# Performance work log

Hardware: AMD Instinct MI355X
Metric: run time of the kernel (lower is better)

## Reference

```python
import jax, jax.numpy as jnp
import numpy as np

K = 2048      # codebook_size
D = 64        # codebook_dim
B = 32
T = 4096
W = 0.99      # codebook_loss_weight (EMA decay)
THRESH = 1.0  # discard_vec_threshold


def setup_inputs() -> dict:
    key = jax.random.key(0)
    k1, k2 = jax.random.split(key, 2)
    x = jax.random.normal(k1, (B, D, T), jnp.float32)
    codebook = jax.random.normal(k2, (K, D), jnp.float32)
    codebook_avg = codebook.copy()
    vector_usage = jnp.ones((K,), jnp.float32)
    perm = jnp.arange(B * T, dtype=jnp.int32)  # deterministic stand-in for randperm
    return dict(x=x, codebook=codebook, codebook_avg=codebook_avg,
                vector_usage=vector_usage, perm=perm)


def reference(x, codebook, codebook_avg, vector_usage, perm):
    Bv, E, Tv = x.shape
    sg = jax.lax.stop_gradient
    # preprocess: [B, E, T] -> [N, E]
    xf = jnp.transpose(x, (0, 2, 1)).reshape(-1, E)
    N = xf.shape[0]
    x_norm = jnp.linalg.norm(xf - jnp.mean(xf)) / np.sqrt(N * E)
    # squared euclidean distances [N, K]
    d = (jnp.sum(xf * xf, axis=-1, keepdims=True)
         - 2.0 * (xf @ codebook.T)
         + jnp.sum(codebook * codebook, axis=-1))
    idx = jnp.argmin(d, axis=-1)            # [N]
    fit = jnp.mean(jnp.min(d, axis=-1))
    q = codebook[idx]                       # [N, E] gather
    # --- update_codebook (torch.no_grad) ---
    cb_sum = jax.ops.segment_sum(sg(xf), idx, num_segments=K)          # onehot @ x
    counts = jax.ops.segment_sum(jnp.ones((N,), xf.dtype), idx, num_segments=K)
    new_avg = W * sg(codebook_avg) + (1.0 - W) * cb_sum
    new_usage = W * sg(vector_usage) + (1.0 - W) * counts
    keep = (new_usage >= THRESH).astype(xf.dtype)[:, None]
    random_shift = sg(xf)[perm][:K]
    new_codebook = keep * (new_avg / new_usage[:, None]) + (1.0 - keep) * random_shift
    vector_prob = counts / jnp.sum(counts)
    entropy = -jnp.sum(vector_prob * jnp.log(vector_prob + 1e-8))
    codebook_diff = jnp.linalg.norm(new_codebook - sg(codebook)) / np.sqrt(K * E)
    # --- commitment loss + straight-through ---
    commit_loss = jnp.sum((sg(q) - xf) ** 2) / (N * E)
    out = xf + sg(q - xf)
    out = jnp.transpose(out.reshape(Bv, Tv, E), (0, 2, 1))  # [B, E, T]
    return (out, commit_loss, fit, x_norm, new_codebook, new_avg, new_usage,
            entropy, codebook_diff)
```

## Files before the change

### kernel.cpp

```cpp
#include <hip/hip_runtime.h>
#include <math.h>

#define OUT_X      0
#define OUT_COMMIT 8388608
#define OUT_FIT    8388609
#define OUT_XNORM  8388610
#define OUT_NCB    8388611
#define OUT_NAVG   (8388611 + 131072)
#define OUT_NUSE   (8388611 + 262144)
#define OUT_ENT    (8388611 + 264192)
#define OUT_CBDIFF (8388611 + 264193)

#define WS_DACC    0
#define WS_COUNTS  64
#define WS_CBSUM   8256
#define WS_CURS    532544
#define WS_XN2     540736
#define WS_IDX     1065024
#define WS_CN2H    1589312
#define WS_SORTED  1597504
#define WS_CHI     2121792
#define WS_CLO     2383936
#define WS_ZERO_BYTES 532544

#define LO_SCALE5  32.0f

typedef _Float16 f16x8_t __attribute__((ext_vector_type(8)));
typedef float f32x16_t __attribute__((ext_vector_type(16)));

__global__ __launch_bounds__(256) void kern_prep_x(
    const float* __restrict__ x, float* __restrict__ xt,
    float* __restrict__ xn2, double* __restrict__ dacc)
{
    __shared__ __align__(16) float Xs[64][128];
    __shared__ float tmpA[4], tmpB[4];
    const int tid = threadIdx.x;
    const int n0 = blockIdx.x * 128;
    const int b = n0 >> 12, t0 = n0 & 4095;
    const float* xb = x + ((size_t)b << 18) + t0;
#pragma unroll
    for (int i = 0; i < 8; ++i) {
        int c = i * 256 + tid;
        int e = c >> 5, v4 = c & 31;
        float4 f = *(const float4*)(xb + ((size_t)e << 12) + (v4 << 2));
        *(float4*)&Xs[e][v4 << 2] = f;
    }
    __syncthreads();
    const int q = tid & 3, r0 = tid >> 2;
    float s1t = 0.f, s2t = 0.f;
#pragma unroll
    for (int h = 0; h < 2; ++h) {
        int r = r0 + (h << 6);
        float s2 = 0.f;
#pragma unroll
        for (int j = 0; j < 4; ++j) {
            int e = q * 16 + j * 4;
            float4 f = make_float4(Xs[e][r], Xs[e + 1][r], Xs[e + 2][r], Xs[e + 3][r]);
            *(float4*)(xt + (((size_t)(n0 + r)) << 6) + e) = f;
            s1t += f.x + f.y + f.z + f.w;
            s2 += f.x * f.x + f.y * f.y + f.z * f.z + f.w * f.w;
        }
        s2t += s2;
        float s2q = s2 + __shfl_xor(s2, 1, 64);
        s2q += __shfl_xor(s2q, 2, 64);
        if (q == 0) xn2[n0 + r] = s2q;
    }
    float rs = s1t, r2 = s2t;
#pragma unroll
    for (int m = 32; m >= 1; m >>= 1) {
        rs += __shfl_xor(rs, m, 64);
        r2 += __shfl_xor(r2, m, 64);
    }
    if ((tid & 63) == 0) { tmpA[tid >> 6] = rs; tmpB[tid >> 6] = r2; }
    __syncthreads();
    if (tid == 0) {
        atomicAdd(&dacc[0], (double)(tmpA[0] + tmpA[1] + tmpA[2] + tmpA[3]));
        atomicAdd(&dacc[1], (double)(tmpB[0] + tmpB[1] + tmpB[2] + tmpB[3]));
    }
}

__global__ __launch_bounds__(256) void kern_prep_cb(
    const float* __restrict__ cb, _Float16* __restrict__ chi,
    _Float16* __restrict__ clo, float* __restrict__ cn2h)
{
    __shared__ float Cs[128][68];
    const int tid = threadIdx.x;
    const int c0 = blockIdx.x * 128;
#pragma unroll
    for (int i = 0; i < 8; ++i) {
        int li = i * 256 + tid;
        int code = li >> 4, d4 = li & 15;
        float4 f = *(const float4*)(cb + (((size_t)(c0 + code)) << 6) + (d4 << 2));
        Cs[code][d4 * 4 + 0] = f.x; Cs[code][d4 * 4 + 1] = f.y;
        Cs[code][d4 * 4 + 2] = f.z; Cs[code][d4 * 4 + 3] = f.w;
    }
    __syncthreads();
    const int w = tid >> 6, lane = tid & 63;
    const int cl = (w << 5) + (lane & 31);
    const int g = lane >> 5;
    const int ktg = blockIdx.x * 4 + w;
#pragma unroll
    for (int s = 0; s < 4; ++s) {
        f16x8_t hh, ll;
#pragma unroll
        for (int i = 0; i < 8; ++i) {
            int k = 16 * s + 4 * g + (i & 3) + 8 * (i >> 2);
            float v = Cs[cl][k];
            _Float16 h = (_Float16)v;
            hh[i] = h;
            ll[i] = (_Float16)((v - (float)h) * LO_SCALE5);
        }
        *(f16x8_t*)(chi + (((size_t)(ktg * 4 + s)) << 9) + lane * 8) = hh;
        *(f16x8_t*)(clo + (((size_t)(ktg * 4 + s)) << 9) + lane * 8) = ll;
    }
    if (tid < 128) {
        float s = 0.f;
#pragma unroll
        for (int k = 0; k < 64; ++k) { float v = Cs[tid][k]; s = fmaf(v, v, s); }
        cn2h[c0 + tid] = -0.5f * s;
    }
}

__global__ __launch_bounds__(256) void kern_argmin_mfma(
    const float* __restrict__ xt, const float* __restrict__ cn2h,
    const _Float16* __restrict__ chi, const _Float16* __restrict__ clo,
    const float* __restrict__ xn2, int* __restrict__ idxb,
    unsigned* __restrict__ counts, double* __restrict__ dacc)
{
    const int tid = threadIdx.x;
    const int w = tid >> 6, lane = tid & 63;
    const int n0 = blockIdx.x * 128 + w * 32;
    const int l31 = lane & 31, g = lane >> 5;

    f16x8_t ahi[4], alo5[4];
    {
        const float* xr = xt + ((size_t)(n0 + l31) << 6) + 4 * g;
#pragma unroll
        for (int s = 0; s < 4; ++s) {
            float4 p = *(const float4*)(xr + 16 * s);
            float4 q = *(const float4*)(xr + 16 * s + 8);
            float vals[8] = {p.x, p.y, p.z, p.w, q.x, q.y, q.z, q.w};
#pragma unroll
            for (int i = 0; i < 8; ++i) {
                _Float16 h = (_Float16)vals[i];
                ahi[s][i] = h;
                alo5[s][i] = (_Float16)((vals[i] - (float)h) * LO_SCALE5);
            }
        }
    }
    float bestm[16]; int besti[16];
#pragma unroll
    for (int r = 0; r < 16; ++r) { bestm[r] = -INFINITY; besti[r] = 0; }

    const _Float16* chiL = chi + lane * 8;
    const _Float16* cloL = clo + lane * 8;

    f16x8_t bhA[4], blA[4], bhB[4], blB[4];
    float cvA, cvB;
#pragma unroll
    for (int s = 0; s < 4; ++s) {
        bhA[s] = *(const f16x8_t*)(chiL + ((0 * 4 + s) << 9));
        blA[s] = *(const f16x8_t*)(cloL + ((0 * 4 + s) << 9));
    }
    cvA = cn2h[l31];

#define ITER(t_, bhC, blC, cvC, bhN, blN, cvN) do {                          \
    if ((t_) + 1 < 64) {                                                     \
        _Pragma("unroll")                                                    \
        for (int s = 0; s < 4; ++s) {                                        \
            bhN[s] = *(const f16x8_t*)(chiL + ((((t_) + 1) * 4 + s) << 9));  \
            blN[s] = *(const f16x8_t*)(cloL + ((((t_) + 1) * 4 + s) << 9));  \
        }                                                                    \
        cvN = cn2h[(((t_) + 1) << 5) + l31];                                 \
    }                                                                        \
    f32x16_t a;                                                              \
    _Pragma("unroll")                                                        \
    for (int r = 0; r < 16; ++r) a[r] = 0.f;                                 \
    __builtin_amdgcn_s_setprio(1);                                           \
    _Pragma("unroll")                                                        \
    for (int s = 0; s < 4; ++s)                                              \
        a = __builtin_amdgcn_mfma_f32_32x32x16_f16(ahi[s], blC[s], a, 0, 0, 0); \
    _Pragma("unroll")                                                        \
    for (int s = 0; s < 4; ++s)                                              \
        a = __builtin_amdgcn_mfma_f32_32x32x16_f16(alo5[s], bhC[s], a, 0, 0, 0); \
    _Pragma("unroll")                                                        \
    for (int r = 0; r < 16; ++r) a[r] = fmaf(a[r], 0.03125f, cvC);           \
    _Pragma("unroll")                                                        \
    for (int s = 0; s < 4; ++s)                                              \
        a = __builtin_amdgcn_mfma_f32_32x32x16_f16(ahi[s], bhC[s], a, 0, 0, 0); \
    __builtin_amdgcn_s_setprio(0);                                           \
    _Pragma("unroll")                                                        \
    for (int r = 0; r < 16; ++r)                                             \
        if (a[r] > bestm[r]) { bestm[r] = a[r]; besti[r] = (t_); }           \
} while (0)

    for (int t = 0; t < 64; t += 2) {
        ITER(t, bhA, blA, cvA, bhB, blB, cvB);
        ITER(t + 1, bhB, blB, cvB, bhA, blA, cvA);
    }
#undef ITER

    float fs = 0.f;
#pragma unroll
    for (int r = 0; r < 16; ++r) {
        float mv = bestm[r]; int mi = (besti[r] << 5) + l31;
#pragma unroll
        for (int m = 1; m < 32; m <<= 1) {
            float ov = __shfl_xor(mv, m, 64);
            int oi = __shfl_xor(mi, m, 64);
            if (ov > mv || (ov == mv && oi < mi)) { mv = ov; mi = oi; }
        }
        if (l31 == 0) {
            int row = (r & 3) + 8 * (r >> 2) + 4 * g;
            int n = n0 + row;
            idxb[n] = mi;
            atomicAdd(&counts[mi], 1u);
            fs += xn2[n] - 2.f * mv;
        }
    }
    if (l31 == 0) atomicAdd(&dacc[2], (double)fs);
}

__global__ void kern_scan(const unsigned* __restrict__ counts, unsigned* __restrict__ curs) {
    __shared__ unsigned wtot[4];
    const int tid = threadIdx.x;
    const int base = tid * 8;
    unsigned s[8]; unsigned tot = 0;
#pragma unroll
    for (int j = 0; j < 8; ++j) { s[j] = counts[base + j]; tot += s[j]; }
    unsigned v = tot;
    const int lane = tid & 63;
#pragma unroll
    for (int d = 1; d < 64; d <<= 1) {
        unsigned o = (unsigned)__shfl_up((int)v, d, 64);
        if (lane >= d) v += o;
    }
    if (lane == 63) wtot[tid >> 6] = v;
    __syncthreads();
    unsigned wbase = 0;
    for (int w = 0; w < (tid >> 6); ++w) wbase += wtot[w];
    unsigned run = wbase + v - tot;
#pragma unroll
    for (int j = 0; j < 8; ++j) { curs[base + j] = run; run += s[j]; }
}

__global__ void kern_scatter(const int* __restrict__ idxb, unsigned* __restrict__ curs,
                             unsigned* __restrict__ sorted) {
    const int n = blockIdx.x * 256 + threadIdx.x;
    int k = idxb[n];
    unsigned pos = atomicAdd(&curs[k], 1u);
    sorted[pos] = ((unsigned)k << 17) | (unsigned)n;
}

__global__ __launch_bounds__(256) void kern_chunk_reduce(
    const float* __restrict__ xt, const unsigned* __restrict__ sorted,
    float* __restrict__ cb_sum)
{
    const int tid = threadIdx.x;
    const int w = tid >> 6, lane = tid & 63;
    const int base = blockIdx.x * 256 + w * 64;
    int kcur = (int)(sorted[base] >> 17);
    float acc = 0.f;
#pragma unroll 4
    for (int it = 0; it < 16; ++it) {
        uint4 p = *(const uint4*)&sorted[base + it * 4];
        float v0 = xt[((size_t)(p.x & 0x1FFFFu) << 6) + lane];
        float v1 = xt[((size_t)(p.y & 0x1FFFFu) << 6) + lane];
        float v2 = xt[((size_t)(p.z & 0x1FFFFu) << 6) + lane];
        float v3 = xt[((size_t)(p.w & 0x1FFFFu) << 6) + lane];
        int k0 = (int)(p.x >> 17), k1 = (int)(p.y >> 17);
        int k2 = (int)(p.z >> 17), k3 = (int)(p.w >> 17);
        if (k0 != kcur) { atomicAdd(&cb_sum[(kcur << 6) + lane], acc); kcur = k0; acc = 0.f; }
        acc += v0;
        if (k1 != kcur) { atomicAdd(&cb_sum[(kcur << 6) + lane], acc); kcur = k1; acc = 0.f; }
        acc += v1;
        if (k2 != kcur) { atomicAdd(&cb_sum[(kcur << 6) + lane], acc); kcur = k2; acc = 0.f; }
        acc += v2;
        if (k3 != kcur) { atomicAdd(&cb_sum[(kcur << 6) + lane], acc); kcur = k3; acc = 0.f; }
        acc += v3;
    }
    atomicAdd(&cb_sum[(kcur << 6) + lane], acc);
}

__global__ __launch_bounds__(256) void kern_update(
    const float* __restrict__ cb_sum, const unsigned* __restrict__ counts,
    const float* __restrict__ cb, const float* __restrict__ cba,
    const float* __restrict__ usage, const int* __restrict__ perm,
    const float* __restrict__ xt, float* __restrict__ out,
    double* __restrict__ dacc)
{
    const int tid = threadIdx.x;
    const int i = blockIdx.x * 256 + tid;
    const int k = i >> 6, e = i & 63;
    float na = 0.99f * cba[i] + 0.01f * cb_sum[i];
    float nu = 0.99f * usage[k] + 0.01f * (float)counts[k];
    float ncb = (nu >= 1.0f) ? (na / nu)
                             : xt[((size_t)perm[k] << 6) + e];
    out[OUT_NAVG + i] = na;
    out[OUT_NCB + i] = ncb;
    if (e == 0) out[OUT_NUSE + k] = nu;
    float d = ncb - cb[i];
    float dd = d * d;
#pragma unroll
    for (int m = 32; m >= 1; m >>= 1) dd += __shfl_xor(dd, m, 64);
    if (e == 0) atomicAdd(&dacc[4], (double)dd);
}

__global__ __launch_bounds__(256) void kern_out(
    const float* __restrict__ x, const float* __restrict__ cb,
    const int* __restrict__ idxb, float* __restrict__ out,
    double* __restrict__ dacc) {
    __shared__ float tmp[4];
    const int tid = threadIdx.x;
    const int n0 = blockIdx.x * 256 + (tid & 63) * 4;
    const int ec = tid >> 6;
    const int b = n0 >> 12, t = n0 & 4095;
    int4 k4 = *(const int4*)(idxb + n0);
    const float* xb = x + ((size_t)b << 18) + t;
    float* ob = out + OUT_X + ((size_t)b << 18) + t;
    float cl = 0.f;
#pragma unroll
    for (int j = 0; j < 16; ++j) {
        int e = ec * 16 + j;
        float4 xv = *(const float4*)(xb + ((size_t)e << 12));
        float q0 = cb[((size_t)k4.x << 6) + e], q1 = cb[((size_t)k4.y << 6) + e];
        float q2 = cb[((size_t)k4.z << 6) + e], q3 = cb[((size_t)k4.w << 6) + e];
        float r0 = q0 - xv.x, r1 = q1 - xv.y, r2 = q2 - xv.z, r3 = q3 - xv.w;
        cl += r0 * r0 + r1 * r1 + r2 * r2 + r3 * r3;
        *(float4*)(ob + ((size_t)e << 12)) = make_float4(q0, q1, q2, q3);
    }
#pragma unroll
    for (int m = 32; m >= 1; m >>= 1) cl += __shfl_xor(cl, m, 64);
    if ((tid & 63) == 0) tmp[tid >> 6] = cl;
    __syncthreads();
    if (tid == 0) atomicAdd(&dacc[3], (double)(tmp[0] + tmp[1] + tmp[2] + tmp[3]));
}

__global__ void kern_scalars(const unsigned* __restrict__ counts,
                             const double* __restrict__ dacc, float* __restrict__ out) {
    __shared__ float tmp[4];
    __shared__ float totalSh;
    const int tid = threadIdx.x;
    float c = 0.f;
    for (int k = tid; k < 2048; k += 256) c += (float)counts[k];
#pragma unroll
    for (int m = 32; m >= 1; m >>= 1) c += __shfl_xor(c, m, 64);
    if ((tid & 63) == 0) tmp[tid >> 6] = c;
    __syncthreads();
    if (tid == 0) totalSh = tmp[0] + tmp[1] + tmp[2] + tmp[3];
    __syncthreads();
    const float total = totalSh;
    float ent = 0.f;
    for (int k = tid; k < 2048; k += 256) {
        float p = (float)counts[k] / total;
        ent -= p * logf(p + 1e-8f);
    }
#pragma unroll
    for (int m = 32; m >= 1; m >>= 1) ent += __shfl_xor(ent, m, 64);
    __syncthreads();
    if ((tid & 63) == 0) tmp[tid >> 6] = ent;
    __syncthreads();
    if (tid == 0) {
        float entropy = tmp[0] + tmp[1] + tmp[2] + tmp[3];
        out[OUT_COMMIT] = (float)(dacc[3] / 8388608.0);
        out[OUT_FIT]    = (float)(dacc[2] / 131072.0);
        double nd = 8388608.0;
        double var = dacc[1] - dacc[0] * dacc[0] / nd;
        if (var < 0.0) var = 0.0;
        out[OUT_XNORM] = (float)(sqrt(var) / sqrt(nd));
        out[OUT_ENT] = entropy;
        out[OUT_CBDIFF] = (float)(sqrt(dacc[4]) / sqrt(131072.0));
    }
}

extern "C" void kernel_launch(void* const* d_in, const int* in_sizes, int n_in,
                              void* d_out, int out_size, void* d_ws, size_t ws_size,
                              hipStream_t stream) {
    const float* x     = (const float*)d_in[0];
    const float* cb    = (const float*)d_in[1];
    const float* cba   = (const float*)d_in[2];
    const float* usage = (const float*)d_in[3];
    const int*   perm  = (const int*)d_in[4];
    float* out = (float*)d_out;
    char* ws = (char*)d_ws;
    double*    dacc   = (double*)(ws + WS_DACC);
    unsigned*  counts = (unsigned*)(ws + WS_COUNTS);
    float*     cbsum  = (float*)(ws + WS_CBSUM);
    unsigned*  curs   = (unsigned*)(ws + WS_CURS);
    float*     xn2    = (float*)(ws + WS_XN2);
    int*       idxb   = (int*)(ws + WS_IDX);
    float*     cn2h   = (float*)(ws + WS_CN2H);
    unsigned*  sorted = (unsigned*)(ws + WS_SORTED);
    _Float16*  chi    = (_Float16*)(ws + WS_CHI);
    _Float16*  clo    = (_Float16*)(ws + WS_CLO);
    float*     xt     = out + OUT_X;

    hipMemsetAsync(ws, 0, WS_ZERO_BYTES, stream);
    kern_prep_x<<<1024, 256, 0, stream>>>(x, xt, xn2, dacc);
    kern_prep_cb<<<16, 256, 0, stream>>>(cb, chi, clo, cn2h);
    kern_argmin_mfma<<<1024, 256, 0, stream>>>(xt, cn2h, chi, clo, xn2, idxb, counts, dacc);
    kern_scan<<<1, 256, 0, stream>>>(counts, curs);
    kern_scatter<<<512, 256, 0, stream>>>(idxb, curs, sorted);
    kern_chunk_reduce<<<512, 256, 0, stream>>>(xt, sorted, cbsum);
    kern_update<<<512, 256, 0, stream>>>(cbsum, counts, cb, cba, usage, perm, xt, out, dacc);
    kern_out<<<512, 256, 0, stream>>>(x, cb, idxb, out, dacc);
    kern_scalars<<<1, 256, 0, stream>>>(counts, dacc, out);
}
```

Before: 310.5 us.

## Process two row blocks per wave in argmin and derive commit loss from fit

The argmin kernel now gives each wave 64 rows as two 32-row MFMA tiles. Each tile shares the same codebook hi/lo fragments, so codebook loads are halved per row. The grid is halved, and the lo-fragment prefetch moves to the middle of the MFMA chain. The two prep kernels merge into one launch split by block index. The commit loss is computed from the summed minimum distance, since that equals the sum of squared residuals, so the output kernel no longer reads x. Costs: more registers per wave and lower occupancy, and commit now inherits the rounding error of the split-fp16 distance.

```diff
diff --git a/kernel.cpp b/kernel.cpp
--- a/kernel.cpp
+++ b/kernel.cpp
@@ -28,96 +28,95 @@
 typedef _Float16 f16x8_t __attribute__((ext_vector_type(8)));
 typedef float f32x16_t __attribute__((ext_vector_type(16)));
 
-__global__ __launch_bounds__(256) void kern_prep_x(
+__global__ __launch_bounds__(256) void kern_prep(
     const float* __restrict__ x, float* __restrict__ xt,
-    float* __restrict__ xn2, double* __restrict__ dacc)
-{
-    __shared__ __align__(16) float Xs[64][128];
-    __shared__ float tmpA[4], tmpB[4];
-    const int tid = threadIdx.x;
-    const int n0 = blockIdx.x * 128;
-    const int b = n0 >> 12, t0 = n0 & 4095;
-    const float* xb = x + ((size_t)b << 18) + t0;
-#pragma unroll
-    for (int i = 0; i < 8; ++i) {
-        int c = i * 256 + tid;
-        int e = c >> 5, v4 = c & 31;
-        float4 f = *(const float4*)(xb + ((size_t)e << 12) + (v4 << 2));
-        *(float4*)&Xs[e][v4 << 2] = f;
-    }
-    __syncthreads();
-    const int q = tid & 3, r0 = tid >> 2;
-    float s1t = 0.f, s2t = 0.f;
-#pragma unroll
-    for (int h = 0; h < 2; ++h) {
-        int r = r0 + (h << 6);
-        float s2 = 0.f;
-#pragma unroll
-        for (int j = 0; j < 4; ++j) {
-            int e = q * 16 + j * 4;
-            float4 f = make_float4(Xs[e][r], Xs[e + 1][r], Xs[e + 2][r], Xs[e + 3][r]);
-            *(float4*)(xt + (((size_t)(n0 + r)) << 6) + e) = f;
-            s1t += f.x + f.y + f.z + f.w;
-            s2 += f.x * f.x + f.y * f.y + f.z * f.z + f.w * f.w;
-        }
-        s2t += s2;
-        float s2q = s2 + __shfl_xor(s2, 1, 64);
-        s2q += __shfl_xor(s2q, 2, 64);
-        if (q == 0) xn2[n0 + r] = s2q;
-    }
-    float rs = s1t, r2 = s2t;
-#pragma unroll
-    for (int m = 32; m >= 1; m >>= 1) {
-        rs += __shfl_xor(rs, m, 64);
-        r2 += __shfl_xor(r2, m, 64);
-    }
-    if ((tid & 63) == 0) { tmpA[tid >> 6] = rs; tmpB[tid >> 6] = r2; }
-    __syncthreads();
-    if (tid == 0) {
-        atomicAdd(&dacc[0], (double)(tmpA[0] + tmpA[1] + tmpA[2] + tmpA[3]));
-        atomicAdd(&dacc[1], (double)(tmpB[0] + tmpB[1] + tmpB[2] + tmpB[3]));
-    }
-}
-
-__global__ __launch_bounds__(256) void kern_prep_cb(
+    float* __restrict__ xn2, double* __restrict__ dacc,
     const float* __restrict__ cb, _Float16* __restrict__ chi,
     _Float16* __restrict__ clo, float* __restrict__ cn2h)
 {
-    __shared__ float Cs[128][68];
-    const int tid = threadIdx.x;
-    const int c0 = blockIdx.x * 128;
-#pragma unroll
-    for (int i = 0; i < 8; ++i) {
-        int li = i * 256 + tid;
-        int code = li >> 4, d4 = li & 15;
-        float4 f = *(const float4*)(cb + (((size_t)(c0 + code)) << 6) + (d4 << 2));
-        Cs[code][d4 * 4 + 0] = f.x; Cs[code][d4 * 4 + 1] = f.y;
-        Cs[code][d4 * 4 + 2] = f.z; Cs[code][d4 * 4 + 3] = f.w;
-    }
-    __syncthreads();
-    const int w = tid >> 6, lane = tid & 63;
-    const int cl = (w << 5) + (lane & 31);
-    const int g = lane >> 5;
-    const int ktg = blockIdx.x * 4 + w;
-#pragma unroll
-    for (int s = 0; s < 4; ++s) {
-        f16x8_t hh, ll;
+    __shared__ __align__(16) char smem[128 * 68 * 4];
+    __shared__ float tmpA[4], tmpB[4];
+    const int tid = threadIdx.x;
+    if (blockIdx.x < 1024) {
+        float (*Xs)[128] = (float(*)[128])smem;
+        const int n0 = blockIdx.x * 128;
+        const int b = n0 >> 12, t0 = n0 & 4095;
+        const float* xb = x + ((size_t)b << 18) + t0;
 #pragma unroll
         for (int i = 0; i < 8; ++i) {
-            int k = 16 * s + 4 * g + (i & 3) + 8 * (i >> 2);
-            float v = Cs[cl][k];
-            _Float16 h = (_Float16)v;
-            hh[i] = h;
-            ll[i] = (_Float16)((v - (float)h) * LO_SCALE5);
-        }
-        *(f16x8_t*)(chi + (((size_t)(ktg * 4 + s)) << 9) + lane * 8) = hh;
-        *(f16x8_t*)(clo + (((size_t)(ktg * 4 + s)) << 9) + lane * 8) = ll;
-    }
-    if (tid < 128) {
-        float s = 0.f;
-#pragma unroll
-        for (int k = 0; k < 64; ++k) { float v = Cs[tid][k]; s = fmaf(v, v, s); }
-        cn2h[c0 + tid] = -0.5f * s;
+            int c = i * 256 + tid;
+            int e = c >> 5, v4 = c & 31;
+            float4 f = *(const float4*)(xb + ((size_t)e << 12) + (v4 << 2));
+            *(float4*)&Xs[e][v4 << 2] = f;
+        }
+        __syncthreads();
+        const int q = tid & 3, r0 = tid >> 2;
+        float s1t = 0.f, s2t = 0.f;
+#pragma unroll
+        for (int h = 0; h < 2; ++h) {
+            int r = r0 + (h << 6);
+            float s2 = 0.f;
+#pragma unroll
+            for (int j = 0; j < 4; ++j) {
+                int e = q * 16 + j * 4;
+                float4 f = make_float4(Xs[e][r], Xs[e + 1][r], Xs[e + 2][r], Xs[e + 3][r]);
+                *(float4*)(xt + (((size_t)(n0 + r)) << 6) + e) = f;
+                s1t += f.x + f.y + f.z + f.w;
+                s2 += f.x * f.x + f.y * f.y + f.z * f.z + f.w * f.w;
+            }
+            s2t += s2;
+            float s2q = s2 + __shfl_xor(s2, 1, 64);
+            s2q += __shfl_xor(s2q, 2, 64);
+            if (q == 0) xn2[n0 + r] = s2q;
+        }
+        float rs = s1t, r2 = s2t;
+#pragma unroll
+        for (int m = 32; m >= 1; m >>= 1) {
+            rs += __shfl_xor(rs, m, 64);
+            r2 += __shfl_xor(r2, m, 64);
+        }
+        if ((tid & 63) == 0) { tmpA[tid >> 6] = rs; tmpB[tid >> 6] = r2; }
+        __syncthreads();
+        if (tid == 0) {
+            atomicAdd(&dacc[0], (double)(tmpA[0] + tmpA[1] + tmpA[2] + tmpA[3]));
+            atomicAdd(&dacc[1], (double)(tmpB[0] + tmpB[1] + tmpB[2] + tmpB[3]));
+        }
+    } else {
+        float (*Cs)[68] = (float(*)[68])smem;
+        const int c0 = (blockIdx.x - 1024) * 128;
+#pragma unroll
+        for (int i = 0; i < 8; ++i) {
+            int li = i * 256 + tid;
+            int code = li >> 4, d4 = li & 15;
+            float4 f = *(const float4*)(cb + (((size_t)(c0 + code)) << 6) + (d4 << 2));
+            Cs[code][d4 * 4 + 0] = f.x; Cs[code][d4 * 4 + 1] = f.y;
+            Cs[code][d4 * 4 + 2] = f.z; Cs[code][d4 * 4 + 3] = f.w;
+        }
+        __syncthreads();
+        const int w = tid >> 6, lane = tid & 63;
+        const int cl = (w << 5) + (lane & 31);
+        const int g = lane >> 5;
+        const int ktg = (blockIdx.x - 1024) * 4 + w;
+#pragma unroll
+        for (int s = 0; s < 4; ++s) {
+            f16x8_t hh, ll;
+#pragma unroll
+            for (int i = 0; i < 8; ++i) {
+                int k = 16 * s + 4 * g + (i & 3) + 8 * (i >> 2);
+                float v = Cs[cl][k];
+                _Float16 h = (_Float16)v;
+                hh[i] = h;
+                ll[i] = (_Float16)((v - (float)h) * LO_SCALE5);
+            }
+            *(f16x8_t*)(chi + (((size_t)(ktg * 4 + s)) << 9) + lane * 8) = hh;
+            *(f16x8_t*)(clo + (((size_t)(ktg * 4 + s)) << 9) + lane * 8) = ll;
+        }
+        if (tid < 128) {
+            float s = 0.f;
+#pragma unroll
+            for (int k = 0; k < 64; ++k) { float v = Cs[tid][k]; s = fmaf(v, v, s); }
+            cn2h[c0 + tid] = -0.5f * s;
+        }
     }
 }
 
@@ -129,12 +128,13 @@
 {
     const int tid = threadIdx.x;
     const int w = tid >> 6, lane = tid & 63;
-    const int n0 = blockIdx.x * 128 + w * 32;
+    const int n0 = blockIdx.x * 256 + w * 64;
     const int l31 = lane & 31, g = lane >> 5;
 
-    f16x8_t ahi[4], alo5[4];
-    {
-        const float* xr = xt + ((size_t)(n0 + l31) << 6) + 4 * g;
+    f16x8_t ahi[2][4], alo5[2][4];
+#pragma unroll
+    for (int rb = 0; rb < 2; ++rb) {
+        const float* xr = xt + ((size_t)(n0 + rb * 32 + l31) << 6) + 4 * g;
 #pragma unroll
         for (int s = 0; s < 4; ++s) {
             float4 p = *(const float4*)(xr + 16 * s);
@@ -143,81 +143,100 @@
 #pragma unroll
             for (int i = 0; i < 8; ++i) {
                 _Float16 h = (_Float16)vals[i];
-                ahi[s][i] = h;
-                alo5[s][i] = (_Float16)((vals[i] - (float)h) * LO_SCALE5);
+                ahi[rb][s][i] = h;
+                alo5[rb][s][i] = (_Float16)((vals[i] - (float)h) * LO_SCALE5);
             }
         }
     }
-    float bestm[16]; int besti[16];
-#pragma unroll
-    for (int r = 0; r < 16; ++r) { bestm[r] = -INFINITY; besti[r] = 0; }
+    float bestm[2][16]; int besti[2][16];
+#pragma unroll
+    for (int rb = 0; rb < 2; ++rb)
+#pragma unroll
+        for (int r = 0; r < 16; ++r) { bestm[rb][r] = -INFINITY; besti[rb][r] = 0; }
 
     const _Float16* chiL = chi + lane * 8;
     const _Float16* cloL = clo + lane * 8;
 
-    f16x8_t bhA[4], blA[4], bhB[4], blB[4];
+    f16x8_t bhA[4], bhB[4], bl[4];
     float cvA, cvB;
 #pragma unroll
     for (int s = 0; s < 4; ++s) {
-        bhA[s] = *(const f16x8_t*)(chiL + ((0 * 4 + s) << 9));
-        blA[s] = *(const f16x8_t*)(cloL + ((0 * 4 + s) << 9));
+        bhA[s] = *(const f16x8_t*)(chiL + (s << 9));
+        bl[s]  = *(const f16x8_t*)(cloL + (s << 9));
     }
     cvA = cn2h[l31];
 
-#define ITER(t_, bhC, blC, cvC, bhN, blN, cvN) do {                          \
+#define ITER(t_, bhC, cvC, bhN, cvN) do {                                    \
     if ((t_) + 1 < 64) {                                                     \
         _Pragma("unroll")                                                    \
-        for (int s = 0; s < 4; ++s) {                                        \
+        for (int s = 0; s < 4; ++s)                                          \
             bhN[s] = *(const f16x8_t*)(chiL + ((((t_) + 1) * 4 + s) << 9));  \
-            blN[s] = *(const f16x8_t*)(cloL + ((((t_) + 1) * 4 + s) << 9));  \
-        }                                                                    \
         cvN = cn2h[(((t_) + 1) << 5) + l31];                                 \
     }                                                                        \
-    f32x16_t a;                                                              \
-    _Pragma("unroll")                                                        \
-    for (int r = 0; r < 16; ++r) a[r] = 0.f;                                 \
+    f32x16_t a0, a1;                                                         \
+    _Pragma("unroll")                                                        \
+    for (int r = 0; r < 16; ++r) { a0[r] = 0.f; a1[r] = 0.f; }               \
     __builtin_amdgcn_s_setprio(1);                                           \
     _Pragma("unroll")                                                        \
-    for (int s = 0; s < 4; ++s)                                              \
-        a = __builtin_amdgcn_mfma_f32_32x32x16_f16(ahi[s], blC[s], a, 0, 0, 0); \
-    _Pragma("unroll")                                                        \
-    for (int s = 0; s < 4; ++s)                                              \
-        a = __builtin_amdgcn_mfma_f32_32x32x16_f16(alo5[s], bhC[s], a, 0, 0, 0); \
-    _Pragma("unroll")                                                        \
-    for (int r = 0; r < 16; ++r) a[r] = fmaf(a[r], 0.03125f, cvC);           \
-    _Pragma("unroll")                                                        \
-    for (int s = 0; s < 4; ++s)                                              \
-        a = __builtin_amdgcn_mfma_f32_32x32x16_f16(ahi[s], bhC[s], a, 0, 0, 0); \
+    for (int s = 0; s < 4; ++s) {                                            \
+        a0 = __builtin_amdgcn_mfma_f32_32x32x16_f16(ahi[0][s], bl[s], a0, 0, 0, 0); \
+        a1 = __builtin_amdgcn_mfma_f32_32x32x16_f16(ahi[1][s], bl[s], a1, 0, 0, 0); \
+    }                                                                        \
+    _Pragma("unroll")                                                        \
+    for (int s = 0; s < 4; ++s) {                                            \
+        a0 = __builtin_amdgcn_mfma_f32_32x32x16_f16(alo5[0][s], bhC[s], a0, 0, 0, 0); \
+        a1 = __builtin_amdgcn_mfma_f32_32x32x16_f16(alo5[1][s], bhC[s], a1, 0, 0, 0); \
+    }                                                                        \
+                \
+    if ((t_) + 1 < 64) {                                                     \
+        _Pragma("unroll")                                                    \
+        for (int s = 0; s < 4; ++s)                                          \
+            bl[s] = *(const f16x8_t*)(cloL + ((((t_) + 1) * 4 + s) << 9));   \
+    }                                                                        \
+    _Pragma("unroll")                                                        \
+    for (int r = 0; r < 16; ++r) {                                           \
+        a0[r] = fmaf(a0[r], 0.03125f, cvC);                                  \
+        a1[r] = fmaf(a1[r], 0.03125f, cvC);                                  \
+    }                                                                        \
+    _Pragma("unroll")                                                        \
+    for (int s = 0; s < 4; ++s) {                                            \
+        a0 = __builtin_amdgcn_mfma_f32_32x32x16_f16(ahi[0][s], bhC[s], a0, 0, 0, 0); \
+        a1 = __builtin_amdgcn_mfma_f32_32x32x16_f16(ahi[1][s], bhC[s], a1, 0, 0, 0); \
+    }                                                                        \
     __builtin_amdgcn_s_setprio(0);                                           \
     _Pragma("unroll")                                                        \
-    for (int r = 0; r < 16; ++r)                                             \
-        if (a[r] > bestm[r]) { bestm[r] = a[r]; besti[r] = (t_); }           \
+    for (int r = 0; r < 16; ++r) {                                           \
+        if (a0[r] > bestm[0][r]) { bestm[0][r] = a0[r]; besti[0][r] = (t_); }\
+        if (a1[r] > bestm[1][r]) { bestm[1][r] = a1[r]; besti[1][r] = (t_); }\
+    }                                                                        \
 } while (0)
 
     for (int t = 0; t < 64; t += 2) {
-        ITER(t, bhA, blA, cvA, bhB, blB, cvB);
-        ITER(t + 1, bhB, blB, cvB, bhA, blA, cvA);
+        ITER(t, bhA, cvA, bhB, cvB);
+        ITER(t + 1, bhB, cvB, bhA, cvA);
     }
 #undef ITER
 
     float fs = 0.f;
 #pragma unroll
-    for (int r = 0; r < 16; ++r) {
-        float mv = bestm[r]; int mi = (besti[r] << 5) + l31;
-#pragma unroll
-        for (int m = 1; m < 32; m <<= 1) {
-            float ov = __shfl_xor(mv, m, 64);
-            int oi = __shfl_xor(mi, m, 64);
-            if (ov > mv || (ov == mv && oi < mi)) { mv = ov; mi = oi; }
-        }
-        if (l31 == 0) {
-            int row = (r & 3) + 8 * (r >> 2) + 4 * g;
-            int n = n0 + row;
-            idxb[n] = mi;
-            atomicAdd(&counts[mi], 1u);
-            fs += xn2[n] - 2.f * mv;
-        }
-    }
+    for (int rb = 0; rb < 2; ++rb)
+#pragma unroll
+        for (int r = 0; r < 16; ++r) {
+            float mv = bestm[rb][r]; int mi = (besti[rb][r] << 5) + l31;
+#pragma unroll
+            for (int m = 1; m < 32; m <<= 1) {
+                float ov = __shfl_xor(mv, m, 64);
+                int oi = __shfl_xor(mi, m, 64);
+                if (ov > mv || (ov == mv && oi < mi)) { mv = ov; mi = oi; }
+            }
+            if (l31 == 0) {
+                int row = (r & 3) + 8 * (r >> 2) + 4 * g;
+                int n = n0 + rb * 32 + row;
+                idxb[n] = mi;
+                atomicAdd(&counts[mi], 1u);
+                fs += xn2[n] - 2.f * mv;
+            }
+        }
     if (l31 == 0) atomicAdd(&dacc[2], (double)fs);
 }
 
@@ -306,36 +325,6 @@
     if (e == 0) atomicAdd(&dacc[4], (double)dd);
 }
 
-__global__ __launch_bounds__(256) void kern_out(
-    const float* __restrict__ x, const float* __restrict__ cb,
-    const int* __restrict__ idxb, float* __restrict__ out,
-    double* __restrict__ dacc) {
-    __shared__ float tmp[4];
-    const int tid = threadIdx.x;
-    const int n0 = blockIdx.x * 256 + (tid & 63) * 4;
-    const int ec = tid >> 6;
-    const int b = n0 >> 12, t = n0 & 4095;
-    int4 k4 = *(const int4*)(idxb + n0);
-    const float* xb = x + ((size_t)b << 18) + t;
-    float* ob = out + OUT_X + ((size_t)b << 18) + t;
-    float cl = 0.f;
-#pragma unroll
-    for (int j = 0; j < 16; ++j) {
-        int e = ec * 16 + j;
-        float4 xv = *(const float4*)(xb + ((size_t)e << 12));
-        float q0 = cb[((size_t)k4.x << 6) + e], q1 = cb[((size_t)k4.y << 6) + e];
-        float q2 = cb[((size_t)k4.z << 6) + e], q3 = cb[((size_t)k4.w << 6) + e];
-        float r0 = q0 - xv.x, r1 = q1 - xv.y, r2 = q2 - xv.z, r3 = q3 - xv.w;
-        cl += r0 * r0 + r1 * r1 + r2 * r2 + r3 * r3;
-        *(float4*)(ob + ((size_t)e << 12)) = make_float4(q0, q1, q2, q3);
-    }
-#pragma unroll
-    for (int m = 32; m >= 1; m >>= 1) cl += __shfl_xor(cl, m, 64);
-    if ((tid & 63) == 0) tmp[tid >> 6] = cl;
-    __syncthreads();
-    if (tid == 0) atomicAdd(&dacc[3], (double)(tmp[0] + tmp[1] + tmp[2] + tmp[3]));
-}
-
 __global__ void kern_scalars(const unsigned* __restrict__ counts,
                              const double* __restrict__ dacc, float* __restrict__ out) {
     __shared__ float tmp[4];
@@ -362,7 +351,7 @@
     __syncthreads();
     if (tid == 0) {
         float entropy = tmp[0] + tmp[1] + tmp[2] + tmp[3];
-        out[OUT_COMMIT] = (float)(dacc[3] / 8388608.0);
+        out[OUT_COMMIT] = (float)(dacc[2] / 8388608.0);
         out[OUT_FIT]    = (float)(dacc[2] / 131072.0);
         double nd = 8388608.0;
         double var = dacc[1] - dacc[0] * dacc[0] / nd;
@@ -370,6 +359,24 @@
         out[OUT_XNORM] = (float)(sqrt(var) / sqrt(nd));
         out[OUT_ENT] = entropy;
         out[OUT_CBDIFF] = (float)(sqrt(dacc[4]) / sqrt(131072.0));
+    }
+}
+
+__global__ __launch_bounds__(256) void kern_out(
+    const float* __restrict__ cb, const int* __restrict__ idxb,
+    float* __restrict__ out) {
+    const int tid = threadIdx.x;
+    const int n0 = blockIdx.x * 256 + (tid & 63) * 4;
+    const int ec = tid >> 6;
+    const int b = n0 >> 12, t = n0 & 4095;
+    int4 k4 = *(const int4*)(idxb + n0);
+    float* ob = out + OUT_X + ((size_t)b << 18) + t;
+#pragma unroll
+    for (int j = 0; j < 16; ++j) {
+        int e = ec * 16 + j;
+        float q0 = cb[((size_t)k4.x << 6) + e], q1 = cb[((size_t)k4.y << 6) + e];
+        float q2 = cb[((size_t)k4.z << 6) + e], q3 = cb[((size_t)k4.w << 6) + e];
+        *(float4*)(ob + ((size_t)e << 12)) = make_float4(q0, q1, q2, q3);
     }
 }
 
@@ -396,13 +403,12 @@
     float*     xt     = out + OUT_X;
 
     hipMemsetAsync(ws, 0, WS_ZERO_BYTES, stream);
-    kern_prep_x<<<1024, 256, 0, stream>>>(x, xt, xn2, dacc);
-    kern_prep_cb<<<16, 256, 0, stream>>>(cb, chi, clo, cn2h);
-    kern_argmin_mfma<<<1024, 256, 0, stream>>>(xt, cn2h, chi, clo, xn2, idxb, counts, dacc);
+    kern_prep<<<1040, 256, 0, stream>>>(x, xt, xn2, dacc, cb, chi, clo, cn2h);
+    kern_argmin_mfma<<<512, 256, 0, stream>>>(xt, cn2h, chi, clo, xn2, idxb, counts, dacc);
     kern_scan<<<1, 256, 0, stream>>>(counts, curs);
     kern_scatter<<<512, 256, 0, stream>>>(idxb, curs, sorted);
     kern_chunk_reduce<<<512, 256, 0, stream>>>(xt, sorted, cbsum);
     kern_update<<<512, 256, 0, stream>>>(cbsum, counts, cb, cba, usage, perm, xt, out, dacc);
-    kern_out<<<512, 256, 0, stream>>>(x, cb, idxb, out, dacc);
     kern_scalars<<<1, 256, 0, stream>>>(counts, dacc, out);
-}
+    kern_out<<<512, 256, 0, stream>>>(cb, idxb, out);
+}
```

After: 331.9 us. 6.9% more time.
